# Performance work log

Measured on AMD Instinct MI355X. Metric: run time of the kernel, lower is better.

The kernel has to match this reference:

```python
import jax, jax.numpy as jnp
import numpy as np


def _qrnn_forward(X, W, b):
    seq_len, batch, d = X.shape
    H = W.shape[0] // 3
    Y = jnp.einsum('sbd,hd->sbh', X, W) + b  # [S,B,3H]
    Z, F, O = jnp.split(Y, 3, axis=2)
    Z = jnp.tanh(Z)
    F = jax.nn.sigmoid(F)

    # ForgetMult with hidden_init=None: h_0 = f_0*z_0; h_t = f_t*z_t + (1-f_t)*h_{t-1}
    # Equivalent to scan from h_{-1} = 0.
    def step(h_prev, fz):
        f_t, z_t = fz
        h = f_t * z_t + (1.0 - f_t) * h_prev
        return h, h

    h0 = jnp.zeros((batch, H), dtype=X.dtype)
    _, C = jax.lax.scan(step, h0, (F, Z))  # [S,B,H]
    Hout = jax.nn.sigmoid(O) * C
    return Hout, C[-1:, :, :]


def setup_inputs() -> dict:
    key = jax.random.key(0)
    k1, k2, k3 = jax.random.split(key, 3)
    S, B, D, Hdim = 1024, 16, 1024, 1024
    X = jax.random.normal(k1, (S, B, D), dtype=jnp.float32)
    W = jax.random.normal(k2, (3 * Hdim, D), dtype=jnp.float32) * (1.0 / np.sqrt(D))
    b = jax.random.normal(k3, (3 * Hdim,), dtype=jnp.float32) * 0.01
    return {"X": X, "W": W, "b": b}


def reference(X, W, b):
    return _qrnn_forward(X, W, b)
```

## Files before the change

kernel.cpp:

```cpp
#include <hip/hip_runtime.h>
#include <hip/hip_bf16.h>
#include <stdint.h>

typedef __bf16 bf16x8 __attribute__((ext_vector_type(8)));
typedef float f32x4 __attribute__((ext_vector_type(4)));

constexpr int S = 1024, Bsz = 16, Hd = 1024;
constexpr int M = S * Bsz;
constexpr int N = 3 * Hd;
constexpr int K = 1024;
constexpr int BM = 128, BN = 128, BK = 32;
constexpr int NCH = 64, CS = S / NCH;
constexpr int BH = Bsz * Hd;
constexpr int EP = 136;

__device__ __forceinline__ float fast_sigmoid(float x) { return 1.0f / (1.0f + __expf(-x)); }
__device__ __forceinline__ float fast_tanh(float x) { return 2.0f / (1.0f + __expf(-2.0f * x)) - 1.0f; }

__device__ __forceinline__ void gld_lds16(const __bf16* g, __bf16* l) {
  __builtin_amdgcn_global_load_lds(
      (const __attribute__((address_space(1))) void*)g,
      (__attribute__((address_space(3))) void*)l,
      16, 0, 0);
}

__global__ void convert_all(const float* __restrict__ X, const float* __restrict__ W,
                            __bf16* __restrict__ Xb, __bf16* __restrict__ Wb) {
  int i = blockIdx.x * blockDim.x + threadIdx.x;
  const float* src; __bf16* dst; int idx;
  if (i < 2097152) { src = X; dst = Xb; idx = i; }
  else             { src = W; dst = Wb; idx = i - 2097152; }
  const float4* s4 = (const float4*)src;
  float4 a = s4[2 * idx], b = s4[2 * idx + 1];
  bf16x8 v;
  v[0] = (__bf16)a.x; v[1] = (__bf16)a.y; v[2] = (__bf16)a.z; v[3] = (__bf16)a.w;
  v[4] = (__bf16)b.x; v[5] = (__bf16)b.y; v[6] = (__bf16)b.z; v[7] = (__bf16)b.w;
  *((bf16x8*)dst + idx) = v;
}

__global__ __launch_bounds__(256) void gemm_act(const __bf16* __restrict__ A,
                                                const __bf16* __restrict__ Bw,
                                                const float* __restrict__ bias,
                                                __bf16* __restrict__ Y) {
  __shared__ __align__(16) __bf16 smem[BM * EP];
  __bf16* As = smem;
  __bf16* Bs = smem + 4096;
  const int t = threadIdx.x;
  const int lane = t & 63;
  const int wave = t >> 6;
  const int wm = wave >> 1, wn = wave & 1;
  const int tn = blockIdx.x % (N / BN);
  const int tm = blockIdx.x / (N / BN);
  const int m0 = tm * BM, n0 = tn * BN;
  const int lrow = lane & 15;
  const int quad = lane >> 4;

  const int srow = t >> 2;
  const int scw = t & 3;
  const __bf16* gA0 = A + (size_t)(m0 + srow) * K + scw * 8;
  const __bf16* gA1 = gA0 + (size_t)64 * K;
  const __bf16* gB0 = Bw + (size_t)(n0 + srow) * K + scw * 8;
  const __bf16* gB1 = gB0 + (size_t)64 * K;
  __bf16* lA0 = As + wave * 512;
  __bf16* lA1 = As + 2048 + wave * 512;
  __bf16* lB0 = Bs + wave * 512;
  __bf16* lB1 = Bs + 2048 + wave * 512;

  f32x4 acc[4][4] = {};

  for (int k0 = 0; k0 < K; k0 += BK) {
    __syncthreads();
    gld_lds16(gA0, lA0);
    gld_lds16(gA1, lA1);
    gld_lds16(gB0, lB0);
    gld_lds16(gB1, lB1);
    gA0 += BK; gA1 += BK; gB0 += BK; gB1 += BK;
    __syncthreads();

    bf16x8 af[4], bfr[4];
#pragma unroll
    for (int mi = 0; mi < 4; ++mi)
      af[mi] = *(const bf16x8*)(&As[(wm * 64 + mi * 16 + lrow) * BK + quad * 8]);
#pragma unroll
    for (int ni = 0; ni < 4; ++ni)
      bfr[ni] = *(const bf16x8*)(&Bs[(wn * 64 + ni * 16 + lrow) * BK + quad * 8]);
#pragma unroll
    for (int mi = 0; mi < 4; ++mi)
#pragma unroll
      for (int ni = 0; ni < 4; ++ni)
        acc[mi][ni] = __builtin_amdgcn_mfma_f32_16x16x32_bf16(af[mi], bfr[ni], acc[mi][ni], 0, 0, 0);
  }

  __syncthreads();
#pragma unroll
  for (int ni = 0; ni < 4; ++ni) {
    int colL = wn * 64 + ni * 16 + lrow;
    int col = n0 + colL;
    float bv = bias[col];
    bool is_tanh = (col < Hd);
#pragma unroll
    for (int mi = 0; mi < 4; ++mi) {
#pragma unroll
      for (int r = 0; r < 4; ++r) {
        int rowL = wm * 64 + mi * 16 + quad * 4 + r;
        float y = acc[mi][ni][r] + bv;
        float v = is_tanh ? fast_tanh(y) : fast_sigmoid(y);
        smem[rowL * EP + colL] = (__bf16)v;
      }
    }
  }
  __syncthreads();
#pragma unroll
  for (int it = 0; it < 8; ++it) {
    int slot = it * 256 + t;
    int rowL = slot >> 4;
    int cw = slot & 15;
    bf16x8 vv = *(const bf16x8*)(&smem[rowL * EP + cw * 8]);
    *(bf16x8*)(&Y[(size_t)(m0 + rowL) * N + n0 + cw * 8]) = vv;
  }
}

__global__ __launch_bounds__(256) void scan_pass1(const __bf16* __restrict__ Y,
                                                  float* __restrict__ Ac,
                                                  float* __restrict__ Bc) {
  int tid = blockIdx.x * 256 + threadIdx.x;
  int c = tid >> 11;
  int r = tid & 2047;
  int bh0 = r << 3;
  int b = bh0 >> 10, h0 = bh0 & (Hd - 1);
  const size_t sstep = (size_t)Bsz * N;
  size_t base0 = (size_t)b * N + h0 + (size_t)(c * CS) * sstep;
  float A[8], Bv[8];
#pragma unroll
  for (int v = 0; v < 8; ++v) { A[v] = 1.0f; Bv[v] = 0.0f; }
#pragma unroll
  for (int j0 = 0; j0 < CS; j0 += 8) {
    bf16x8 zv[8], fv[8];
#pragma unroll
    for (int j = 0; j < 8; ++j) {
      size_t base = base0 + (size_t)(j0 + j) * sstep;
      zv[j] = *(const bf16x8*)(Y + base);
      fv[j] = *(const bf16x8*)(Y + base + Hd);
    }
#pragma unroll
    for (int j = 0; j < 8; ++j) {
#pragma unroll
      for (int v = 0; v < 8; ++v) {
        float z = (float)zv[j][v], f = (float)fv[j][v];
        float a = 1.0f - f;
        Bv[v] = fmaf(a, Bv[v], f * z);
        A[v] *= a;
      }
    }
  }
  int ob = c * BH + bh0;
  f32x4 a0, a1, b0, b1;
#pragma unroll
  for (int v = 0; v < 4; ++v) { a0[v] = A[v]; a1[v] = A[v + 4]; b0[v] = Bv[v]; b1[v] = Bv[v + 4]; }
  *(f32x4*)(Ac + ob) = a0;
  *(f32x4*)(Ac + ob + 4) = a1;
  *(f32x4*)(Bc + ob) = b0;
  *(f32x4*)(Bc + ob + 4) = b1;
}

__global__ __launch_bounds__(256) void scan_pass2(const float* __restrict__ Ac,
                                                  const float* __restrict__ Bc,
                                                  float* __restrict__ hin,
                                                  float* __restrict__ clast) {
  int bh = blockIdx.x * 256 + threadIdx.x;
  float h = 0.0f;
#pragma unroll 8
  for (int c = 0; c < NCH; ++c) {
    hin[c * BH + bh] = h;
    h = fmaf(Ac[c * BH + bh], h, Bc[c * BH + bh]);
  }
  clast[bh] = h;
}

__global__ __launch_bounds__(256) void scan_pass3(const __bf16* __restrict__ Y,
                                                  const float* __restrict__ hin,
                                                  float* __restrict__ hout) {
  int tid = blockIdx.x * 256 + threadIdx.x;
  int c = tid >> 11;
  int r = tid & 2047;
  int bh0 = r << 3;
  int b = bh0 >> 10, h0 = bh0 & (Hd - 1);
  const size_t sstep = (size_t)Bsz * N;
  size_t base0 = (size_t)b * N + h0 + (size_t)(c * CS) * sstep;
  size_t obase0 = (size_t)b * Hd + h0 + (size_t)(c * CS) * BH;
  float hp[8];
  {
    f32x4 h04 = *(const f32x4*)(hin + c * BH + bh0);
    f32x4 h14 = *(const f32x4*)(hin + c * BH + bh0 + 4);
#pragma unroll
    for (int v = 0; v < 4; ++v) { hp[v] = h04[v]; hp[v + 4] = h14[v]; }
  }
#pragma unroll
  for (int j0 = 0; j0 < CS; j0 += 8) {
    bf16x8 zv[8], fv[8], ov[8];
#pragma unroll
    for (int j = 0; j < 8; ++j) {
      size_t base = base0 + (size_t)(j0 + j) * sstep;
      zv[j] = *(const bf16x8*)(Y + base);
      fv[j] = *(const bf16x8*)(Y + base + Hd);
      ov[j] = *(const bf16x8*)(Y + base + 2 * Hd);
    }
#pragma unroll
    for (int j = 0; j < 8; ++j) {
      f32x4 o0, o1;
#pragma unroll
      for (int v = 0; v < 8; ++v) {
        float z = (float)zv[j][v], f = (float)fv[j][v], o = (float)ov[j][v];
        hp[v] = fmaf(f, z - hp[v], hp[v]);
        float out = o * hp[v];
        if (v < 4) o0[v] = out; else o1[v - 4] = out;
      }
      size_t ob = obase0 + (size_t)(j0 + j) * BH;
      *(f32x4*)(hout + ob) = o0;
      *(f32x4*)(hout + ob + 4) = o1;
    }
  }
}

extern "C" void kernel_launch(void* const* d_in, const int* in_sizes, int n_in,
                              void* d_out, int out_size, void* d_ws, size_t ws_size,
                              hipStream_t stream) {
  const float* X = (const float*)d_in[0];
  const float* W = (const float*)d_in[1];
  const float* bias = (const float*)d_in[2];
  float* out = (float*)d_out;

  char* ws = (char*)d_ws;
  __bf16* Xb = (__bf16*)ws;
  __bf16* Wb = (__bf16*)(ws + 33554432);
  __bf16* Yv = (__bf16*)(ws + 39845888);
  float* Ac = (float*)(ws + 39845888 + 100663296);
  float* Bc = Ac + NCH * BH;
  float* hin = Bc + NCH * BH;

  convert_all<<<9728, 256, 0, stream>>>(X, W, Xb, Wb);

  dim3 ggrid((M / BM) * (N / BN));
  dim3 vgrid(NCH * BH / 8 / 256);
  gemm_act<<<ggrid, 256, 0, stream>>>(Xb, Wb, bias, Yv);
  scan_pass1<<<vgrid, 256, 0, stream>>>(Yv, Ac, Bc);
  scan_pass2<<<BH / 256, 256, 0, stream>>>(Ac, Bc, hin, out + 16777216);
  scan_pass3<<<vgrid, 256, 0, stream>>>(Yv, hin, out);
}
```

Baseline: 310.1 us.

## Double-buffer GEMM LDS tiles to overlap global loads with MFMA

Splits the GEMM's shared memory into two A/B tile buffers, prefetching the next K-slice with global_load_lds while MFMAs run on the current one. This drops one of the two barriers per iteration and is meant to hide global-load latency behind compute. It relies on the single remaining __syncthreads also waiting for the async LDS loads to complete. If the compiler does not insert a vmcnt wait there, tiles could be read before they are fully written.

```diff
diff --git a/kernel.cpp b/kernel.cpp
--- a/kernel.cpp
+++ b/kernel.cpp
@@ -43,8 +43,10 @@
                                                 const float* __restrict__ bias,
                                                 __bf16* __restrict__ Y) {
   __shared__ __align__(16) __bf16 smem[BM * EP];
-  __bf16* As = smem;
-  __bf16* Bs = smem + 4096;
+  __bf16* As0 = smem;
+  __bf16* Bs0 = smem + 4096;
+  __bf16* As1 = smem + 8192;
+  __bf16* Bs1 = smem + 12288;
   const int t = threadIdx.x;
   const int lane = t & 63;
   const int wave = t >> 6;
@@ -61,29 +63,53 @@
   const __bf16* gA1 = gA0 + (size_t)64 * K;
   const __bf16* gB0 = Bw + (size_t)(n0 + srow) * K + scw * 8;
   const __bf16* gB1 = gB0 + (size_t)64 * K;
-  __bf16* lA0 = As + wave * 512;
-  __bf16* lA1 = As + 2048 + wave * 512;
-  __bf16* lB0 = Bs + wave * 512;
-  __bf16* lB1 = Bs + 2048 + wave * 512;
+  const int wofs = wave * 512;
 
   f32x4 acc[4][4] = {};
 
-  for (int k0 = 0; k0 < K; k0 += BK) {
+  gld_lds16(gA0, As0 + wofs);
+  gld_lds16(gA1, As0 + 2048 + wofs);
+  gld_lds16(gB0, Bs0 + wofs);
+  gld_lds16(gB1, Bs0 + 2048 + wofs);
+  gA0 += BK; gA1 += BK; gB0 += BK; gB1 += BK;
+  __syncthreads();
+
+  __bf16* curA = As0; __bf16* curB = Bs0;
+  __bf16* nxtA = As1; __bf16* nxtB = Bs1;
+
+  for (int kt = 0; kt < K / BK - 1; ++kt) {
+    gld_lds16(gA0, nxtA + wofs);
+    gld_lds16(gA1, nxtA + 2048 + wofs);
+    gld_lds16(gB0, nxtB + wofs);
+    gld_lds16(gB1, nxtB + 2048 + wofs);
+    gA0 += BK; gA1 += BK; gB0 += BK; gB1 += BK;
+
+    bf16x8 af[4], bfr[4];
+#pragma unroll
+    for (int mi = 0; mi < 4; ++mi)
+      af[mi] = *(const bf16x8*)(&curA[(wm * 64 + mi * 16 + lrow) * BK + quad * 8]);
+#pragma unroll
+    for (int ni = 0; ni < 4; ++ni)
+      bfr[ni] = *(const bf16x8*)(&curB[(wn * 64 + ni * 16 + lrow) * BK + quad * 8]);
+#pragma unroll
+    for (int mi = 0; mi < 4; ++mi)
+#pragma unroll
+      for (int ni = 0; ni < 4; ++ni)
+        acc[mi][ni] = __builtin_amdgcn_mfma_f32_16x16x32_bf16(af[mi], bfr[ni], acc[mi][ni], 0, 0, 0);
+
     __syncthreads();
-    gld_lds16(gA0, lA0);
-    gld_lds16(gA1, lA1);
-    gld_lds16(gB0, lB0);
-    gld_lds16(gB1, lB1);
-    gA0 += BK; gA1 += BK; gB0 += BK; gB1 += BK;
-    __syncthreads();
-
+    __bf16* tA = curA; curA = nxtA; nxtA = tA;
+    __bf16* tB = curB; curB = nxtB; nxtB = tB;
+  }
+
+  {
     bf16x8 af[4], bfr[4];
 #pragma unroll
     for (int mi = 0; mi < 4; ++mi)
-      af[mi] = *(const bf16x8*)(&As[(wm * 64 + mi * 16 + lrow) * BK + quad * 8]);
+      af[mi] = *(const bf16x8*)(&curA[(wm * 64 + mi * 16 + lrow) * BK + quad * 8]);
 #pragma unroll
     for (int ni = 0; ni < 4; ++ni)
-      bfr[ni] = *(const bf16x8*)(&Bs[(wn * 64 + ni * 16 + lrow) * BK + quad * 8]);
+      bfr[ni] = *(const bf16x8*)(&curB[(wn * 64 + ni * 16 + lrow) * BK + quad * 8]);
 #pragma unroll
     for (int mi = 0; mi < 4; ++mi)
 #pragma unroll
```

After: 314.6 us. About the same (+1.4%).

## Pipeline GEMM K-loop with four-stage LDS ring buffer and async loads

Applied to the files above, without the earlier changes.

Replaces the single-buffered K loop (two barriers per step) with a 4-slot LDS ring, where global-to-LDS loads run two stages ahead. Manual vmcnt waits and bare s_barrier replace __syncthreads. The aim is to hide global load latency behind MFMA work. The change grows LDS use to 64KB and relies on hand-counted vmcnt values. Reusing slot 0 two stages after it was read depends on the barrier ordering, which risks a race if waves fall out of sync.

```diff
diff --git a/kernel.cpp b/kernel.cpp
--- a/kernel.cpp
+++ b/kernel.cpp
@@ -42,9 +42,7 @@
                                                 const __bf16* __restrict__ Bw,
                                                 const float* __restrict__ bias,
                                                 __bf16* __restrict__ Y) {
-  __shared__ __align__(16) __bf16 smem[BM * EP];
-  __bf16* As = smem;
-  __bf16* Bs = smem + 4096;
+  __shared__ __align__(16) __bf16 smem[32768];
   const int t = threadIdx.x;
   const int lane = t & 63;
   const int wave = t >> 6;
@@ -61,35 +59,57 @@
   const __bf16* gA1 = gA0 + (size_t)64 * K;
   const __bf16* gB0 = Bw + (size_t)(n0 + srow) * K + scw * 8;
   const __bf16* gB1 = gB0 + (size_t)64 * K;
-  __bf16* lA0 = As + wave * 512;
-  __bf16* lA1 = As + 2048 + wave * 512;
-  __bf16* lB0 = Bs + wave * 512;
-  __bf16* lB1 = Bs + 2048 + wave * 512;
+  const int wofs = wave * 512;
 
   f32x4 acc[4][4] = {};
 
-  for (int k0 = 0; k0 < K; k0 += BK) {
-    __syncthreads();
-    gld_lds16(gA0, lA0);
-    gld_lds16(gA1, lA1);
-    gld_lds16(gB0, lB0);
-    gld_lds16(gB1, lB1);
-    gA0 += BK; gA1 += BK; gB0 += BK; gB1 += BK;
-    __syncthreads();
-
-    bf16x8 af[4], bfr[4];
-#pragma unroll
-    for (int mi = 0; mi < 4; ++mi)
-      af[mi] = *(const bf16x8*)(&As[(wm * 64 + mi * 16 + lrow) * BK + quad * 8]);
-#pragma unroll
-    for (int ni = 0; ni < 4; ++ni)
-      bfr[ni] = *(const bf16x8*)(&Bs[(wn * 64 + ni * 16 + lrow) * BK + quad * 8]);
-#pragma unroll
-    for (int mi = 0; mi < 4; ++mi)
-#pragma unroll
-      for (int ni = 0; ni < 4; ++ni)
-        acc[mi][ni] = __builtin_amdgcn_mfma_f32_16x16x32_bf16(af[mi], bfr[ni], acc[mi][ni], 0, 0, 0);
-  }
+#define STAGE4(OFS)                                                       \
+  {                                                                       \
+    gld_lds16(gA0, smem + (OFS) + wofs);                                  \
+    gld_lds16(gA1, smem + (OFS) + 2048 + wofs);                           \
+    gld_lds16(gB0, smem + (OFS) + 4096 + wofs);                           \
+    gld_lds16(gB1, smem + (OFS) + 6144 + wofs);                           \
+    gA0 += BK; gA1 += BK; gB0 += BK; gB1 += BK;                           \
+  }
+
+#define CMP(OFS)                                                          \
+  {                                                                       \
+    bf16x8 af[4], bfr[4];                                                 \
+    _Pragma("unroll")                                                     \
+    for (int mi = 0; mi < 4; ++mi)                                        \
+      af[mi] = *(const bf16x8*)(&smem[(OFS) + (wm * 64 + mi * 16 + lrow) * BK + quad * 8]); \
+    _Pragma("unroll")                                                     \
+    for (int ni = 0; ni < 4; ++ni)                                        \
+      bfr[ni] = *(const bf16x8*)(&smem[(OFS) + 4096 + (wn * 64 + ni * 16 + lrow) * BK + quad * 8]); \
+    _Pragma("unroll")                                                     \
+    for (int mi = 0; mi < 4; ++mi)                                        \
+      _Pragma("unroll")                                                   \
+      for (int ni = 0; ni < 4; ++ni)                                      \
+        acc[mi][ni] = __builtin_amdgcn_mfma_f32_16x16x32_bf16(af[mi], bfr[ni], acc[mi][ni], 0, 0, 0); \
+  }
+
+#define WAITV(NN) asm volatile("s_waitcnt vmcnt(" #NN ")" ::: "memory")
+#define BAR() __builtin_amdgcn_s_barrier()
+
+  STAGE4(0);
+  STAGE4(8192);
+
+#pragma unroll 1
+  for (int g = 0; g < 7; ++g) {
+    STAGE4(16384); WAITV(8); BAR(); CMP(0);
+    STAGE4(24576); WAITV(8); BAR(); CMP(8192);
+    STAGE4(0);     WAITV(8); BAR(); CMP(16384);
+    STAGE4(8192);  WAITV(8); BAR(); CMP(24576);
+  }
+  STAGE4(16384); WAITV(8); BAR(); CMP(0);
+  STAGE4(24576); WAITV(8); BAR(); CMP(8192);
+  WAITV(4); BAR(); CMP(16384);
+  WAITV(0); BAR(); CMP(24576);
+
+#undef STAGE4
+#undef CMP
+#undef WAITV
+#undef BAR
 
   __syncthreads();
 #pragma unroll
```

Measured after the change: 303.1 us. -2.2%, faster.
